# Kernel optimization log

Measured on AMD Instinct MI355X. Metric: run time of the kernel, lower is better.

Reference implementation:

```python
import jax, jax.numpy as jnp
import numpy as np

N_USERS = 50000
N_ITEMS = 100000
N_GROUPS = 20000
D = 128
NNZ_U = 1000000
NNZ_I = 2000000
NNZ_F = 3000000


def setup_inputs() -> dict:
    key = jax.random.key(0)
    ks = jax.random.split(key, 14)
    user_emb = jax.random.normal(ks[0], (N_USERS, D), jnp.float32)
    item_emb = jax.random.normal(ks[1], (N_ITEMS, D), jnp.float32)
    group_emb = jax.random.normal(ks[2], (N_GROUPS, D), jnp.float32)
    # user hypergraph incidence [N_GROUPS, N_USERS] in COO
    u_rows = jax.random.randint(ks[3], (NNZ_U,), 0, N_GROUPS)
    u_cols = jax.random.randint(ks[4], (NNZ_U,), 0, N_USERS)
    u_vals = jax.random.uniform(ks[5], (NNZ_U,), jnp.float32)
    # item hypergraph incidence [N_GROUPS, N_ITEMS] in COO
    i_rows = jax.random.randint(ks[6], (NNZ_I,), 0, N_GROUPS)
    i_cols = jax.random.randint(ks[7], (NNZ_I,), 0, N_ITEMS)
    i_vals = jax.random.uniform(ks[8], (NNZ_I,), jnp.float32)
    # full hypergraph [N_USERS+N_ITEMS, N_GROUPS] in COO
    f_rows = jax.random.randint(ks[9], (NNZ_F,), 0, N_USERS + N_ITEMS)
    f_cols = jax.random.randint(ks[10], (NNZ_F,), 0, N_GROUPS)
    f_vals = jax.random.uniform(ks[11], (NNZ_F,), jnp.float32)
    # nn.Linear(2D, D): weight [D, 2D], bias [D]
    W_agg = jax.random.normal(ks[12], (D, 2 * D), jnp.float32) * 0.05
    b_agg = jnp.zeros((D,), jnp.float32)
    return dict(user_emb=user_emb, item_emb=item_emb, group_emb=group_emb,
                u_rows=u_rows, u_cols=u_cols, u_vals=u_vals,
                i_rows=i_rows, i_cols=i_cols, i_vals=i_vals,
                f_rows=f_rows, f_cols=f_cols, f_vals=f_vals,
                W_agg=W_agg, b_agg=b_agg)


def _spmm(rows, cols, vals, dense, num_rows):
    # sparse[rows, cols]=vals (COO) @ dense -> [num_rows, d]
    return jax.ops.segment_sum(vals[:, None] * dense[cols], rows, num_segments=num_rows)


def reference(user_emb, item_emb, group_emb,
              u_rows, u_cols, u_vals,
              i_rows, i_cols, i_vals,
              f_rows, f_cols, f_vals,
              W_agg, b_agg):
    user_msg = _spmm(u_rows, u_cols, u_vals, user_emb, N_GROUPS)   # [G, D]
    item_msg = _spmm(i_rows, i_cols, i_vals, item_emb, N_GROUPS)   # [G, D]
    msg = jnp.concatenate([user_msg, item_msg], axis=1) @ W_agg.T + b_agg  # [G, D]
    norm_emb = _spmm(f_rows, f_cols, f_vals, msg, N_USERS + N_ITEMS)       # [U+I, D]
    return (norm_emb, msg)
```

## Files before the change

### kernel.cpp

```cpp
#include <hip/hip_runtime.h>
#include <hip/hip_bf16.h>
#include <stdint.h>

#define N_USERS  50000
#define N_ITEMS  100000
#define N_GROUPS 20000
#define DIM      128
#define TWO_DIM  256
#define N_FULL   (N_USERS + N_ITEMS)

#define NBU  625
#define NBI  1250
#define NBF  2344
#define NBT  (NBU + NBI + NBF)
#define CAP  2048

#define TILE_E 8192
#define NT     736
#define NT_PER_XCD 92

__device__ __forceinline__ unsigned bf16_rne(float f)
{
    unsigned u = __float_as_uint(f);
    return (u + 0x7FFFu + ((u >> 16) & 1u)) >> 16;
}
__device__ __forceinline__ unsigned bf16_pack(float a, float b)
{
    return bf16_rne(a) | (bf16_rne(b) << 16);
}

__global__ __launch_bounds__(256) void spmm_atomic(
    const int* __restrict__ rows, const int* __restrict__ cols,
    const float* __restrict__ vals, const float* __restrict__ dense,
    float* __restrict__ out, int nnz)
{
    long long t = (long long)blockIdx.x * blockDim.x + threadIdx.x;
    int e    = (int)(t >> 5);
    int lane = (int)(t & 31);
    if (e >= nnz) return;
    int   r = rows[e];
    int   c = cols[e];
    float v = vals[e];
    float4 x = ((const float4*)(dense + (size_t)c * DIM))[lane];
    float* dst = out + (size_t)r * DIM + lane * 4;
    atomicAdd(dst + 0, v * x.x);
    atomicAdd(dst + 1, v * x.y);
    atomicAdd(dst + 2, v * x.z);
    atomicAdd(dst + 3, v * x.w);
}

__device__ __forceinline__ int bucket_of_nt(long long t,
    const int* __restrict__ u_rows, int nnz_u,
    const int* __restrict__ i_rows, int nnz_i,
    const int* __restrict__ f_rows)
{
    if (t < nnz_u)                          return __builtin_nontemporal_load(u_rows + t) >> 5;
    else if (t < (long long)nnz_u + nnz_i)  return NBU + (__builtin_nontemporal_load(i_rows + (t - nnz_u)) >> 4);
    else                                    return NBU + NBI + (__builtin_nontemporal_load(f_rows + (t - nnz_u - nnz_i)) >> 6);
}

__global__ __launch_bounds__(512) void hist_tiles(
    const int* __restrict__ u_rows, int nnz_u,
    const int* __restrict__ i_rows, int nnz_i,
    const int* __restrict__ f_rows, int nnz_f,
    unsigned short* __restrict__ M,
    const float4* __restrict__ cu_src, uint2* __restrict__ cu_dst, int n4u,
    const float4* __restrict__ ci_src, uint2* __restrict__ ci_dst, int n4i)
{
    __shared__ int h[NBT];
    int tid = threadIdx.x;
    for (int i = tid; i < NBT; i += 512) h[i] = 0;
    __syncthreads();
    int t = (blockIdx.x & 7) * NT_PER_XCD + (blockIdx.x >> 3);
    long long total = (long long)nnz_u + nnz_i + nnz_f;
    long long base  = (long long)t * TILE_E;
    for (int j = tid; j < TILE_E; j += 512) {
        long long e = base + j;
        if (e >= total) break;
        atomicAdd(&h[bucket_of_nt(e, u_rows, nnz_u, i_rows, nnz_i, f_rows)], 1);
    }
    __syncthreads();
    unsigned short* Mrow = M + (size_t)t * NBT;
    for (int i = tid; i < NBT; i += 512) Mrow[i] = (unsigned short)h[i];

    if (cu_dst) {
        int stride = gridDim.x * 512;
        for (int i = blockIdx.x * 512 + tid; i < n4u; i += stride) {
            float4 v = cu_src[i];
            cu_dst[i] = make_uint2(bf16_pack(v.x, v.y), bf16_pack(v.z, v.w));
        }
        for (int i = blockIdx.x * 512 + tid; i < n4i; i += stride) {
            float4 v = ci_src[i];
            ci_dst[i] = make_uint2(bf16_pack(v.x, v.y), bf16_pack(v.z, v.w));
        }
    }
}

__global__ __launch_bounds__(64) void tile_prefix(
    unsigned short* __restrict__ M, int* __restrict__ btot)
{
    int b = blockIdx.x * 64 + threadIdx.x;
    if (b >= NBT) return;
    int run = 0;
#pragma unroll 1
    for (int t = 0; t < NT; t += 4) {
        size_t i0 = (size_t)(t + 0) * NBT + b;
        size_t i1 = (size_t)(t + 1) * NBT + b;
        size_t i2 = (size_t)(t + 2) * NBT + b;
        size_t i3 = (size_t)(t + 3) * NBT + b;
        int v0 = M[i0], v1 = M[i1], v2 = M[i2], v3 = M[i3];
        M[i0] = (unsigned short)run; run += v0;
        M[i1] = (unsigned short)run; run += v1;
        M[i2] = (unsigned short)run; run += v2;
        M[i3] = (unsigned short)run; run += v3;
    }
    btot[b] = run;
}

__global__ __launch_bounds__(256) void scan_buckets(
    const int* __restrict__ btot, int* __restrict__ bptr)
{
    __shared__ int wsum[4];
    __shared__ int s_carry;
    int tid = threadIdx.x, lane = tid & 63, wave = tid >> 6;
    if (tid == 0) s_carry = 0;
    __syncthreads();
    for (int base = 0; base < NBT; base += 256) {
        int b = base + tid;
        int x = (b < NBT) ? btot[b] : 0;
        int incl = x;
#pragma unroll
        for (int off = 1; off < 64; off <<= 1) {
            int y = __shfl_up(incl, off, 64);
            if (lane >= off) incl += y;
        }
        if (lane == 63) wsum[wave] = incl;
        __syncthreads();
        int waveOff = 0;
        for (int w = 0; w < wave; ++w) waveOff += wsum[w];
        int carry = s_carry;
        int ex = carry + waveOff + incl - x;
        if (b < NBT) bptr[b] = ex;
        __syncthreads();
        if (tid == 255) s_carry = carry + waveOff + incl;
        __syncthreads();
    }
    if (tid == 0) bptr[NBT] = s_carry;
}

__global__ __launch_bounds__(512) void scatter_tiles(
    const int* __restrict__ u_rows, const int* __restrict__ u_cols,
    const float* __restrict__ u_vals, int nnz_u,
    const int* __restrict__ i_rows, const int* __restrict__ i_cols,
    const float* __restrict__ i_vals, int nnz_i,
    const int* __restrict__ f_rows, const int* __restrict__ f_cols,
    const float* __restrict__ f_vals, int nnz_f,
    const unsigned short* __restrict__ M, const int* __restrict__ bptr,
    uint2* __restrict__ pack)
{
    __shared__ int cur[NBT];
    int tid = threadIdx.x;
    int t = (blockIdx.x & 7) * NT_PER_XCD + (blockIdx.x >> 3);
    const unsigned short* Mrow = M + (size_t)t * NBT;
    for (int i = tid; i < NBT; i += 512) cur[i] = bptr[i] + (int)Mrow[i];
    __syncthreads();
    long long total = (long long)nnz_u + nnz_i + nnz_f;
    long long base  = (long long)t * TILE_E;
    for (int j = tid; j < TILE_E; j += 512) {
        long long e = base + j;
        if (e >= total) break;
        int b, lrow, col; float v;
        if (e < nnz_u) {
            int k = (int)e; int r = __builtin_nontemporal_load(u_rows + k);
            b = r >> 5; lrow = r & 31;
            col = __builtin_nontemporal_load(u_cols + k);
            v   = __builtin_nontemporal_load(u_vals + k);
        } else if (e < (long long)nnz_u + nnz_i) {
            int k = (int)(e - nnz_u); int r = __builtin_nontemporal_load(i_rows + k);
            b = NBU + (r >> 4); lrow = r & 15;
            col = __builtin_nontemporal_load(i_cols + k);
            v   = __builtin_nontemporal_load(i_vals + k);
        } else {
            int k = (int)(e - nnz_u - nnz_i); int r = __builtin_nontemporal_load(f_rows + k);
            b = NBU + NBI + (r >> 6); lrow = r & 63;
            col = __builtin_nontemporal_load(f_cols + k);
            v   = __builtin_nontemporal_load(f_vals + k);
        }
        int p = atomicAdd(&cur[b], 1);
        pack[p] = make_uint2(((unsigned)lrow << 17) | (unsigned)col, __float_as_uint(v));
    }
}

template<bool BF16>
__device__ __forceinline__ void edge_fma(
    const void* __restrict__ dense, unsigned col, int sl, float v, float4& a)
{
    if constexpr (BF16) {
        uint2 q = ((const uint2*)dense)[(size_t)col * 32 + sl];
        float x0 = __uint_as_float(q.x << 16);
        float x1 = __uint_as_float(q.x & 0xFFFF0000u);
        float x2 = __uint_as_float(q.y << 16);
        float x3 = __uint_as_float(q.y & 0xFFFF0000u);
        a.x = fmaf(v, x0, a.x); a.y = fmaf(v, x1, a.y);
        a.z = fmaf(v, x2, a.z); a.w = fmaf(v, x3, a.w);
    } else {
        float4 x = ((const float4*)dense)[(size_t)col * 32 + sl];
        a.x = fmaf(v, x.x, a.x); a.y = fmaf(v, x.y, a.y);
        a.z = fmaf(v, x.z, a.z); a.w = fmaf(v, x.w, a.w);
    }
}

template<bool BF16>
__global__ __launch_bounds__(512) void gather_buckets(
    const int* __restrict__ bptr, const uint2* __restrict__ pack,
    const void* __restrict__ denseA, float* __restrict__ outA,
    int nbA, int rowsA, int nrowsA, int baseA,
    const void* __restrict__ denseB, float* __restrict__ outB,
    int rowsB, int nrowsB, int baseB)
{
    __shared__ uint2 sR[CAP];
    __shared__ uint2 sE[CAP];
    __shared__ int   h[64];
    __shared__ int   o[65];

    const void* dense; float* out; int rowsPB, nrows, lb, bid;
    if ((int)blockIdx.x < nbA) {
        dense = denseA; out = outA; rowsPB = rowsA; nrows = nrowsA;
        lb = blockIdx.x; bid = baseA + lb;
    } else {
        dense = denseB; out = outB; rowsPB = rowsB; nrows = nrowsB;
        lb = blockIdx.x - nbA; bid = baseB + lb;
    }
    int tid = threadIdx.x;
    if (tid < 64) h[tid] = 0;

    int p0 = bptr[bid], p1 = bptr[bid + 1];
    int cnt = p1 - p0;
    if (cnt > CAP) cnt = CAP;

    for (int j = tid; j < cnt; j += 512) sR[j] = pack[p0 + j];
    __syncthreads();

    for (int j = tid; j < cnt; j += 512)
        atomicAdd(&h[sR[j].x >> 17], 1);
    __syncthreads();

    if (tid < 64) {
        int x = (tid < rowsPB) ? h[tid] : 0;
        int incl = x;
#pragma unroll
        for (int off = 1; off < 64; off <<= 1) {
            int y = __shfl_up(incl, off, 64);
            if ((tid & 63) >= off) incl += y;
        }
        o[tid + 1] = incl;
        if (tid == 0) o[0] = 0;
        h[tid] = incl - x;
    }
    __syncthreads();

    for (int j = tid; j < cnt; j += 512) {
        uint2 e = sR[j];
        int r = e.x >> 17;
        int p = atomicAdd(&h[r], 1);
        sE[p] = make_uint2(e.x & 0x1FFFF, e.y);
    }
    __syncthreads();

    int wave = tid >> 6, lane = tid & 63, half = lane >> 5, sl = lane & 31;
    float4* out4 = (float4*)out;
    for (int r = wave; r < rowsPB; r += 8) {
        int s = o[r], epos = o[r + 1];
        float4 a0 = make_float4(0.f, 0.f, 0.f, 0.f);
        float4 a1 = a0, a2 = a0, a3 = a0, a4 = a0, a5 = a0, a6 = a0, a7 = a0;
        for (int base = s; base < epos; base += 16) {
            int j0 = base +  0 + half, j1 = base +  2 + half;
            int j2 = base +  4 + half, j3 = base +  6 + half;
            int j4 = base +  8 + half, j5 = base + 10 + half;
            int j6 = base + 12 + half, j7 = base + 14 + half;
            if (j0 < epos) { uint2 e = sE[j0]; edge_fma<BF16>(dense, e.x, sl, __uint_as_float(e.y), a0); }
            if (j1 < epos) { uint2 e = sE[j1]; edge_fma<BF16>(dense, e.x, sl, __uint_as_float(e.y), a1); }
            if (j2 < epos) { uint2 e = sE[j2]; edge_fma<BF16>(dense, e.x, sl, __uint_as_float(e.y), a2); }
            if (j3 < epos) { uint2 e = sE[j3]; edge_fma<BF16>(dense, e.x, sl, __uint_as_float(e.y), a3); }
            if (j4 < epos) { uint2 e = sE[j4]; edge_fma<BF16>(dense, e.x, sl, __uint_as_float(e.y), a4); }
            if (j5 < epos) { uint2 e = sE[j5]; edge_fma<BF16>(dense, e.x, sl, __uint_as_float(e.y), a5); }
            if (j6 < epos) { uint2 e = sE[j6]; edge_fma<BF16>(dense, e.x, sl, __uint_as_float(e.y), a6); }
            if (j7 < epos) { uint2 e = sE[j7]; edge_fma<BF16>(dense, e.x, sl, __uint_as_float(e.y), a7); }
        }
        float4 acc;
        acc.x = ((a0.x + a1.x) + (a2.x + a3.x)) + ((a4.x + a5.x) + (a6.x + a7.x));
        acc.y = ((a0.y + a1.y) + (a2.y + a3.y)) + ((a4.y + a5.y) + (a6.y + a7.y));
        acc.z = ((a0.z + a1.z) + (a2.z + a3.z)) + ((a4.z + a5.z) + (a6.z + a7.z));
        acc.w = ((a0.w + a1.w) + (a2.w + a3.w)) + ((a4.w + a5.w) + (a6.w + a7.w));
        acc.x += __shfl_xor(acc.x, 32, 64);
        acc.y += __shfl_xor(acc.y, 32, 64);
        acc.z += __shfl_xor(acc.z, 32, 64);
        acc.w += __shfl_xor(acc.w, 32, 64);
        int row = lb * rowsPB + r;
        if (half == 0 && row < nrows)
            out4[(size_t)row * 32 + sl] = acc;
    }
}

__global__ __launch_bounds__(256) void dense_agg(
    const float* __restrict__ um, const float* __restrict__ im,
    const float* __restrict__ W, const float* __restrict__ b,
    float* __restrict__ msg, uint4* __restrict__ msgb)
{
    __shared__ float As[32][68];
    __shared__ float Ws[64][132];

    int tid = threadIdx.x;
    int tx  = tid & 15;
    int ty  = tid >> 4;
    int rowBase = blockIdx.x * 32;

    float acc[2][8];
#pragma unroll
    for (int i = 0; i < 2; ++i)
#pragma unroll
        for (int j = 0; j < 8; ++j) acc[i][j] = 0.f;

    for (int kc = 0; kc < 4; ++kc) {
        int k0 = kc * 64;
        const float* Asrc = (k0 < DIM) ? um : im;
        int kOff = (k0 < DIM) ? k0 : (k0 - DIM);

#pragma unroll
        for (int l = 0; l < 2; ++l) {
            int idx = tid + l * 256;
            int r   = idx >> 4;
            int kq  = idx & 15;
            int gRow = rowBase + r;
            float4 v = make_float4(0.f, 0.f, 0.f, 0.f);
            if (gRow < N_GROUPS)
                v = *(const float4*)(Asrc + (size_t)gRow * DIM + kOff + kq * 4);
            *(float4*)&As[r][kq * 4] = v;
        }
#pragma unroll
        for (int l = 0; l < 8; ++l) {
            int idx = tid + l * 256;
            int d   = idx >> 4;
            int kq  = idx & 15;
            float4 v = *(const float4*)(W + (size_t)d * TWO_DIM + k0 + kq * 4);
            Ws[kq * 4 + 0][d] = v.x;
            Ws[kq * 4 + 1][d] = v.y;
            Ws[kq * 4 + 2][d] = v.z;
            Ws[kq * 4 + 3][d] = v.w;
        }
        __syncthreads();

        int ty2 = ty * 2;
        int tx8 = tx * 8;
#pragma unroll 8
        for (int k = 0; k < 64; ++k) {
            float a0 = As[ty2 + 0][k];
            float a1 = As[ty2 + 1][k];
            float4 w0 = *(const float4*)&Ws[k][tx8];
            float4 w1 = *(const float4*)&Ws[k][tx8 + 4];
            acc[0][0] = fmaf(a0, w0.x, acc[0][0]);
            acc[0][1] = fmaf(a0, w0.y, acc[0][1]);
            acc[0][2] = fmaf(a0, w0.z, acc[0][2]);
            acc[0][3] = fmaf(a0, w0.w, acc[0][3]);
            acc[0][4] = fmaf(a0, w1.x, acc[0][4]);
            acc[0][5] = fmaf(a0, w1.y, acc[0][5]);
            acc[0][6] = fmaf(a0, w1.z, acc[0][6]);
            acc[0][7] = fmaf(a0, w1.w, acc[0][7]);
            acc[1][0] = fmaf(a1, w0.x, acc[1][0]);
            acc[1][1] = fmaf(a1, w0.y, acc[1][1]);
            acc[1][2] = fmaf(a1, w0.z, acc[1][2]);
            acc[1][3] = fmaf(a1, w0.w, acc[1][3]);
            acc[1][4] = fmaf(a1, w1.x, acc[1][4]);
            acc[1][5] = fmaf(a1, w1.y, acc[1][5]);
            acc[1][6] = fmaf(a1, w1.z, acc[1][6]);
            acc[1][7] = fmaf(a1, w1.w, acc[1][7]);
        }
        __syncthreads();
    }

    int d0 = tx * 8;
    float4 bv0 = *(const float4*)(b + d0);
    float4 bv1 = *(const float4*)(b + d0 + 4);
#pragma unroll
    for (int i = 0; i < 2; ++i) {
        int gRow = rowBase + ty * 2 + i;
        if (gRow < N_GROUPS) {
            float4 o0 = make_float4(acc[i][0] + bv0.x, acc[i][1] + bv0.y,
                                    acc[i][2] + bv0.z, acc[i][3] + bv0.w);
            float4 o1 = make_float4(acc[i][4] + bv1.x, acc[i][5] + bv1.y,
                                    acc[i][6] + bv1.z, acc[i][7] + bv1.w);
            *(float4*)(msg + (size_t)gRow * DIM + d0)     = o0;
            *(float4*)(msg + (size_t)gRow * DIM + d0 + 4) = o1;
            if (msgb) {
                uint4 pb;
                pb.x = bf16_pack(o0.x, o0.y);
                pb.y = bf16_pack(o0.z, o0.w);
                pb.z = bf16_pack(o1.x, o1.y);
                pb.w = bf16_pack(o1.z, o1.w);
                msgb[(size_t)gRow * 16 + tx] = pb;
            }
        }
    }
}

extern "C" void kernel_launch(void* const* d_in, const int* in_sizes, int n_in,
                              void* d_out, int out_size, void* d_ws, size_t ws_size,
                              hipStream_t stream)
{
    const float* user_emb = (const float*)d_in[0];
    const float* item_emb = (const float*)d_in[1];
    const int*   u_rows = (const int*)d_in[3];
    const int*   u_cols = (const int*)d_in[4];
    const float* u_vals = (const float*)d_in[5];
    const int*   i_rows = (const int*)d_in[6];
    const int*   i_cols = (const int*)d_in[7];
    const float* i_vals = (const float*)d_in[8];
    const int*   f_rows = (const int*)d_in[9];
    const int*   f_cols = (const int*)d_in[10];
    const float* f_vals = (const float*)d_in[11];
    const float* W      = (const float*)d_in[12];
    const float* bias   = (const float*)d_in[13];

    int nnz_u = in_sizes[3];
    int nnz_i = in_sizes[6];
    int nnz_f = in_sizes[9];
    long long nnz_tot = (long long)nnz_u + nnz_i + nnz_f;

    float* out  = (float*)d_out;
    float* norm = out;
    float* msg  = out + (size_t)N_FULL * DIM;

    float* um = norm;
    float* im = norm + (size_t)N_GROUPS * DIM;

    auto ceil16 = [](size_t b) { return (b + 15) & ~(size_t)15; };
    size_t need = 0;
    size_t o_M    = need; need += ceil16((size_t)NT * NBT * 2);
    size_t o_btot = need; need += ceil16((size_t)NBT * 4);
    size_t o_bptr = need; need += ceil16((size_t)(NBT + 1) * 4);
    size_t o_pack = need; need += ceil16((size_t)nnz_tot * 8);
    size_t need_base = need;
    size_t o_ebf  = need; need += ceil16((size_t)(N_USERS + N_ITEMS) * DIM * 2);
    size_t o_msgb = need; need += ceil16((size_t)N_GROUPS * DIM * 2);
    size_t need_bf16 = need;

    if (ws_size >= need_base && nnz_tot <= (long long)NT * TILE_E) {
        bool use_bf16 = (ws_size >= need_bf16);
        uint8_t* ws = (uint8_t*)d_ws;
        unsigned short* M = (unsigned short*)(ws + o_M);
        int*   btot = (int*)(ws + o_btot);
        int*   bptr = (int*)(ws + o_bptr);
        uint2* pack = (uint2*)(ws + o_pack);
        uint2* ubf  = (uint2*)(ws + o_ebf);
        uint2* ibf  = ubf + (size_t)N_USERS * 32;
        uint4* msgb = (uint4*)(ws + o_msgb);

        hist_tiles<<<NT, 512, 0, stream>>>(
            u_rows, nnz_u, i_rows, nnz_i, f_rows, nnz_f, M,
            use_bf16 ? (const float4*)user_emb : nullptr,
            use_bf16 ? ubf : nullptr, N_USERS * (DIM / 4),
            use_bf16 ? (const float4*)item_emb : nullptr,
            use_bf16 ? ibf : nullptr, N_ITEMS * (DIM / 4));

        tile_prefix<<<(NBT + 63) / 64, 64, 0, stream>>>(M, btot);

        scan_buckets<<<1, 256, 0, stream>>>(btot, bptr);

        scatter_tiles<<<NT, 512, 0, stream>>>(
            u_rows, u_cols, u_vals, nnz_u,
            i_rows, i_cols, i_vals, nnz_i,
            f_rows, f_cols, f_vals, nnz_f,
            M, bptr, pack);

        if (use_bf16) {
            gather_buckets<true><<<NBU + NBI, 512, 0, stream>>>(
                bptr, pack,
                ubf, um, NBU, 32, N_GROUPS, 0,
                ibf, im, 16, N_GROUPS, NBU);

            dense_agg<<<(N_GROUPS + 31) / 32, 256, 0, stream>>>(
                um, im, W, bias, msg, msgb);

            gather_buckets<true><<<NBF, 512, 0, stream>>>(
                bptr, pack,
                msgb, norm, NBF, 64, N_FULL, NBU + NBI,
                msgb, norm, 64, N_FULL, NBU + NBI);
        } else {
            gather_buckets<false><<<NBU + NBI, 512, 0, stream>>>(
                bptr, pack,
                user_emb, um, NBU, 32, N_GROUPS, 0,
                item_emb, im, 16, N_GROUPS, NBU);

            dense_agg<<<(N_GROUPS + 31) / 32, 256, 0, stream>>>(
                um, im, W, bias, msg, nullptr);

            gather_buckets<false><<<NBF, 512, 0, stream>>>(
                bptr, pack,
                msg, norm, NBF, 64, N_FULL, NBU + NBI,
                msg, norm, 64, N_FULL, NBU + NBI);
        }
    } else {
        hipMemsetAsync(norm, 0, (size_t)N_FULL * DIM * sizeof(float), stream);
        auto spmm_blocks = [](int nnz) {
            return (unsigned)(((long long)nnz * 32 + 255) / 256);
        };
        spmm_atomic<<<spmm_blocks(nnz_u), 256, 0, stream>>>(
            u_rows, u_cols, u_vals, user_emb, um, nnz_u);
        spmm_atomic<<<spmm_blocks(nnz_i), 256, 0, stream>>>(
            i_rows, i_cols, i_vals, item_emb, im, nnz_i);
        dense_agg<<<(N_GROUPS + 31) / 32, 256, 0, stream>>>(
            um, im, W, bias, msg, nullptr);
        hipMemsetAsync(norm, 0, (size_t)2 * N_GROUPS * DIM * sizeof(float), stream);
        spmm_atomic<<<spmm_blocks(nnz_f), 256, 0, stream>>>(
            f_rows, f_cols, f_vals, msg, norm, nnz_f);
    }
}
```

Before: 725.0 us.

## Sub-bin gather edges by column range so waves sweep dense rows together

Each block now sorts its bucket's edges into (row, column-chunk) bins instead of per-row bins. All waves walk column chunk by chunk, holding accumulators for several rows in registers, so concurrent gathers hit a narrow slice of the dense matrix for better cache locality. The exchange is extra registers (RPW rows times two float4 accumulators), a bigger block-wide scan, and less memory-level parallelism per row: two edges in flight per half-wave instead of eight.

```diff
diff --git a/kernel.cpp b/kernel.cpp
--- a/kernel.cpp
+++ b/kernel.cpp
@@ -210,7 +210,7 @@
     }
 }
 
-template<bool BF16>
+template<bool BF16, int NC, int RPW>
 __global__ __launch_bounds__(512) void gather_buckets(
     const int* __restrict__ bptr, const uint2* __restrict__ pack,
     const void* __restrict__ denseA, float* __restrict__ outA,
@@ -218,10 +218,12 @@
     const void* __restrict__ denseB, float* __restrict__ outB,
     int rowsB, int nrowsB, int baseB)
 {
+    constexpr int NBIN = 64 * NC;
     __shared__ uint2 sR[CAP];
     __shared__ uint2 sE[CAP];
-    __shared__ int   h[64];
-    __shared__ int   o[65];
+    __shared__ int   h[NBIN];
+    __shared__ int   off[NBIN + 1];
+    __shared__ int   wsum[8];
 
     const void* dense; float* out; int rowsPB, nrows, lb, bid;
     if ((int)blockIdx.x < nbA) {
@@ -232,7 +234,8 @@
         lb = blockIdx.x - nbA; bid = baseB + lb;
     }
     int tid = threadIdx.x;
-    if (tid < 64) h[tid] = 0;
+    int lane = tid & 63, wave = tid >> 6;
+    for (int i = tid; i < NBIN; i += 512) h[i] = 0;
 
     int p0 = bptr[bid], p1 = bptr[bid + 1];
     int cnt = p1 - p0;
@@ -241,64 +244,86 @@
     for (int j = tid; j < cnt; j += 512) sR[j] = pack[p0 + j];
     __syncthreads();
 
+    auto bin_of = [](unsigned ex) {
+        int c = (NC > 1) ? (int)((ex & 0x1FFFFu) >> 13) : 0;
+        return (int)(ex >> 17) * NC + c;
+    };
+
     for (int j = tid; j < cnt; j += 512)
-        atomicAdd(&h[sR[j].x >> 17], 1);
-    __syncthreads();
-
-    if (tid < 64) {
-        int x = (tid < rowsPB) ? h[tid] : 0;
-        int incl = x;
-#pragma unroll
-        for (int off = 1; off < 64; off <<= 1) {
-            int y = __shfl_up(incl, off, 64);
-            if ((tid & 63) >= off) incl += y;
-        }
-        o[tid + 1] = incl;
-        if (tid == 0) o[0] = 0;
-        h[tid] = incl - x;
+        atomicAdd(&h[bin_of(sR[j].x)], 1);
+    __syncthreads();
+
+    {
+        int x0 = 0, x1 = 0;
+        if (2 * tid < NBIN) { x0 = h[2 * tid]; x1 = h[2 * tid + 1]; }
+        int s = x0 + x1;
+        int incl = s;
+#pragma unroll
+        for (int o = 1; o < 64; o <<= 1) {
+            int y = __shfl_up(incl, o, 64);
+            if (lane >= o) incl += y;
+        }
+        if (lane == 63) wsum[wave] = incl;
+        __syncthreads();
+        int waveOff = 0;
+        for (int w = 0; w < wave; ++w) waveOff += wsum[w];
+        int start = waveOff + incl - s;
+        if (2 * tid < NBIN) {
+            off[2 * tid]     = start;      h[2 * tid]     = start;
+            off[2 * tid + 1] = start + x0; h[2 * tid + 1] = start + x0;
+        }
+        if (tid == 511) off[NBIN] = waveOff + incl;
     }
     __syncthreads();
 
     for (int j = tid; j < cnt; j += 512) {
         uint2 e = sR[j];
-        int r = e.x >> 17;
-        int p = atomicAdd(&h[r], 1);
+        int p = atomicAdd(&h[bin_of(e.x)], 1);
         sE[p] = make_uint2(e.x & 0x1FFFF, e.y);
     }
     __syncthreads();
 
-    int wave = tid >> 6, lane = tid & 63, half = lane >> 5, sl = lane & 31;
+    int half = lane >> 5, sl = lane & 31;
+    float4 aA[RPW], aB[RPW];
+#pragma unroll
+    for (int rl = 0; rl < RPW; ++rl) {
+        aA[rl] = make_float4(0.f, 0.f, 0.f, 0.f);
+        aB[rl] = make_float4(0.f, 0.f, 0.f, 0.f);
+    }
+#pragma unroll 1
+    for (int c = 0; c < NC; ++c) {
+#pragma unroll
+        for (int rl = 0; rl < RPW; ++rl) {
+            int row = wave + rl * 8;
+            if (row < rowsPB) {
+                int s0 = off[row * NC + c], e2 = off[row * NC + c + 1];
+                for (int base = s0; base < e2; base += 4) {
+                    int j0 = base + half, j1 = base + 2 + half;
+                    if (j0 < e2) { uint2 ed = sE[j0]; edge_fma<BF16>(dense, ed.x, sl, __uint_as_float(ed.y), aA[rl]); }
+                    if (j1 < e2) { uint2 ed = sE[j1]; edge_fma<BF16>(dense, ed.x, sl, __uint_as_float(ed.y), aB[rl]); }
+                }
+            }
+        }
+    }
+
     float4* out4 = (float4*)out;
-    for (int r = wave; r < rowsPB; r += 8) {
-        int s = o[r], epos = o[r + 1];
-        float4 a0 = make_float4(0.f, 0.f, 0.f, 0.f);
-        float4 a1 = a0, a2 = a0, a3 = a0, a4 = a0, a5 = a0, a6 = a0, a7 = a0;
-        for (int base = s; base < epos; base += 16) {
-            int j0 = base +  0 + half, j1 = base +  2 + half;
-            int j2 = base +  4 + half, j3 = base +  6 + half;
-            int j4 = base +  8 + half, j5 = base + 10 + half;
-            int j6 = base + 12 + half, j7 = base + 14 + half;
-            if (j0 < epos) { uint2 e = sE[j0]; edge_fma<BF16>(dense, e.x, sl, __uint_as_float(e.y), a0); }
-            if (j1 < epos) { uint2 e = sE[j1]; edge_fma<BF16>(dense, e.x, sl, __uint_as_float(e.y), a1); }
-            if (j2 < epos) { uint2 e = sE[j2]; edge_fma<BF16>(dense, e.x, sl, __uint_as_float(e.y), a2); }
-            if (j3 < epos) { uint2 e = sE[j3]; edge_fma<BF16>(dense, e.x, sl, __uint_as_float(e.y), a3); }
-            if (j4 < epos) { uint2 e = sE[j4]; edge_fma<BF16>(dense, e.x, sl, __uint_as_float(e.y), a4); }
-            if (j5 < epos) { uint2 e = sE[j5]; edge_fma<BF16>(dense, e.x, sl, __uint_as_float(e.y), a5); }
-            if (j6 < epos) { uint2 e = sE[j6]; edge_fma<BF16>(dense, e.x, sl, __uint_as_float(e.y), a6); }
-            if (j7 < epos) { uint2 e = sE[j7]; edge_fma<BF16>(dense, e.x, sl, __uint_as_float(e.y), a7); }
-        }
-        float4 acc;
-        acc.x = ((a0.x + a1.x) + (a2.x + a3.x)) + ((a4.x + a5.x) + (a6.x + a7.x));
-        acc.y = ((a0.y + a1.y) + (a2.y + a3.y)) + ((a4.y + a5.y) + (a6.y + a7.y));
-        acc.z = ((a0.z + a1.z) + (a2.z + a3.z)) + ((a4.z + a5.z) + (a6.z + a7.z));
-        acc.w = ((a0.w + a1.w) + (a2.w + a3.w)) + ((a4.w + a5.w) + (a6.w + a7.w));
-        acc.x += __shfl_xor(acc.x, 32, 64);
-        acc.y += __shfl_xor(acc.y, 32, 64);
-        acc.z += __shfl_xor(acc.z, 32, 64);
-        acc.w += __shfl_xor(acc.w, 32, 64);
-        int row = lb * rowsPB + r;
-        if (half == 0 && row < nrows)
-            out4[(size_t)row * 32 + sl] = acc;
+#pragma unroll
+    for (int rl = 0; rl < RPW; ++rl) {
+        int row = wave + rl * 8;
+        if (row < rowsPB) {
+            float4 acc;
+            acc.x = aA[rl].x + aB[rl].x;
+            acc.y = aA[rl].y + aB[rl].y;
+            acc.z = aA[rl].z + aB[rl].z;
+            acc.w = aA[rl].w + aB[rl].w;
+            acc.x += __shfl_xor(acc.x, 32, 64);
+            acc.y += __shfl_xor(acc.y, 32, 64);
+            acc.z += __shfl_xor(acc.z, 32, 64);
+            acc.w += __shfl_xor(acc.w, 32, 64);
+            int orow = lb * rowsPB + row;
+            if (half == 0 && orow < nrows)
+                out4[(size_t)orow * 32 + sl] = acc;
+        }
     }
 }
 
@@ -473,7 +498,7 @@
             M, bptr, pack);
 
         if (use_bf16) {
-            gather_buckets<true><<<NBU + NBI, 512, 0, stream>>>(
+            gather_buckets<true, 16, 4><<<NBU + NBI, 512, 0, stream>>>(
                 bptr, pack,
                 ubf, um, NBU, 32, N_GROUPS, 0,
                 ibf, im, 16, N_GROUPS, NBU);
@@ -481,12 +506,12 @@
             dense_agg<<<(N_GROUPS + 31) / 32, 256, 0, stream>>>(
                 um, im, W, bias, msg, msgb);
 
-            gather_buckets<true><<<NBF, 512, 0, stream>>>(
+            gather_buckets<true, 4, 8><<<NBF, 512, 0, stream>>>(
                 bptr, pack,
                 msgb, norm, NBF, 64, N_FULL, NBU + NBI,
                 msgb, norm, 64, N_FULL, NBU + NBI);
         } else {
-            gather_buckets<false><<<NBU + NBI, 512, 0, stream>>>(
+            gather_buckets<false, 16, 4><<<NBU + NBI, 512, 0, stream>>>(
                 bptr, pack,
                 user_emb, um, NBU, 32, N_GROUPS, 0,
                 item_emb, im, 16, N_GROUPS, NBU);
@@ -494,7 +519,7 @@
             dense_agg<<<(N_GROUPS + 31) / 32, 256, 0, stream>>>(
                 um, im, W, bias, msg, nullptr);
 
-            gather_buckets<false><<<NBF, 512, 0, stream>>>(
+            gather_buckets<false, 4, 8><<<NBF, 512, 0, stream>>>(
                 bptr, pack,
                 msg, norm, NBF, 64, N_FULL, NBU + NBI,
                 msg, norm, 64, N_FULL, NBU + NBI);
```

Result: slower. 799.1 us (+10.2%).
